# Optimization experiments

Hardware: AMD Instinct MI355X
Metric: run time of the kernel (lower is better)

Reference implementation:

```python
import jax, jax.numpy as jnp
import numpy as np

N, E, F_IN, H, D = 50000, 800000, 128, 4, 32


def setup_inputs() -> dict:
    key = jax.random.key(0)
    k_x, k_e, k_w, k_al, k_ar = jax.random.split(key, 5)
    x = jax.random.normal(k_x, (N, F_IN), dtype=jnp.float32)
    edge_index = jax.random.randint(k_e, (2, E), 0, N, dtype=jnp.int32).astype(jnp.int64)
    # xavier-uniform-like scales
    s_w = float(np.sqrt(6.0 / (F_IN + H * D)))
    s_a = float(np.sqrt(6.0 / (D + 1)))
    W = jax.random.uniform(k_w, (F_IN, H * D), jnp.float32, -s_w, s_w)
    att_l = jax.random.uniform(k_al, (H, D), jnp.float32, -s_a, s_a)
    att_r = jax.random.uniform(k_ar, (H, D), jnp.float32, -s_a, s_a)
    bias = jnp.zeros((H * D,), jnp.float32)
    return {"x": x, "edge_index": edge_index, "W": W, "att_l": att_l, "att_r": att_r, "bias": bias}


def reference(x, edge_index, W, att_l, att_r, bias):
    num_nodes = x.shape[0]
    n_heads, head_dim = att_l.shape
    h = (x @ W).reshape(num_nodes, n_heads, head_dim)          # [N,H,D]
    alpha_l = jnp.einsum('nhd,hd->nh', h, att_l)               # [N,H]
    alpha_r = jnp.einsum('nhd,hd->nh', h, att_r)               # [N,H]
    from_idx, to_idx = edge_index[0], edge_index[1]
    att = alpha_l[from_idx] + alpha_r[to_idx]                  # [E,H]
    att = jax.nn.leaky_relu(att, negative_slope=0.2)
    # segment softmax over edges grouped by destination node (shift by global
    # per-head max, exactly as the source's _softmax effectively does)
    att = att - jax.lax.stop_gradient(jnp.max(att, axis=0, keepdims=True))
    ex = jnp.exp(att)                                          # [E,H]
    denom = jax.ops.segment_sum(ex, to_idx, num_segments=num_nodes)  # [N,H]
    att_n = ex / (denom[to_idx] + 1e-9)                        # [E,H]
    # scatter-weighted aggregation: out[n] = sum_{e: to=n} att[e] * h[from[e]]
    msgs = att_n[:, :, None] * h[from_idx]                     # [E,H,D]
    out = jax.ops.segment_sum(msgs, to_idx, num_segments=num_nodes)  # [N,H,D]
    out = out.reshape(num_nodes, n_heads * head_dim) + bias
    return out
```

## Files before the change

kernel.cpp:

```cpp
#include <hip/hip_runtime.h>
#include <cstdint>

#define N_NODES 50000
#define N_EDGES 800000
#define F_IN    128
#define N_HEADS 4
#define HEAD_DIM 32
#define F_OUT   128

#define NBUCK   391
#define NPB     128
#define KA_GRID 512
#define EPB     1563
#define EPB_PAD 1568
#define REC_CAP 2560
#define STAGE_CAP REC_CAP
#define NSTRIP  (N_NODES / 16)
#define NGEMM   ((NSTRIP + 3) / 4)

typedef unsigned int uint32;
typedef unsigned short ushort;
typedef __attribute__((ext_vector_type(8))) short short8v;
typedef __attribute__((ext_vector_type(4))) float float4v;

typedef __attribute__((address_space(1))) const ushort gushort;
typedef __attribute__((address_space(3))) ushort lushort;

__device__ __forceinline__ ushort f2bf(float f) {
    uint32 u = __float_as_uint(f);
    return (ushort)((u + 0x7FFFu + ((u >> 16) & 1u)) >> 16);
}


__device__ __forceinline__ int block_scan_excl_256(int v, int* p_total)
{
    const int t = threadIdx.x, lane = t & 63, wv = t >> 6;
    int incl = v;
#pragma unroll
    for (int d = 1; d < 64; d <<= 1) {
        int u = __shfl_up(incl, d);
        if (lane >= d) incl += u;
    }
    __shared__ int wsum[4];
    if (lane == 63) wsum[wv] = incl;
    __syncthreads();
    int woff = 0;
#pragma unroll
    for (int j = 0; j < 4; ++j) {
        int s = wsum[j];
        if (j < wv) woff += s;
    }
    if (p_total) *p_total = wsum[0] + wsum[1] + wsum[2] + wsum[3];
    __syncthreads();
    return woff + incl - v;
}

__global__ __launch_bounds__(256) void k_prep(const float* __restrict__ W,
    ushort* __restrict__ WTF)
{
    const int id = blockIdx.x * 256 + threadIdx.x;
    if (id >= 32 * 64) return;
    const int tile = id >> 6, l = id & 63;
    const int q = l >> 4, c15 = l & 15;
    const int nt = tile >> 2, kt = tile & 3;
    short8v hv, lv;
#pragma unroll
    for (int j = 0; j < 8; ++j) {
        const int k = kt * 32 + q * 8 + j;
        const float w = W[k * F_OUT + nt * 16 + c15];
        const ushort hi = f2bf(w);
        const float hif = __uint_as_float((uint32)hi << 16);
        hv[j] = (short)hi;
        lv[j] = (short)f2bf(w - hif);
    }
    *(short8v*)&WTF[tile * 512 + l * 8]         = hv;
    *(short8v*)&WTF[16384 + tile * 512 + l * 8] = lv;
}

__global__ __launch_bounds__(256, 2) void k_bin_gemm(
    const int* __restrict__ ei, const float* __restrict__ x,
    const ushort* __restrict__ WTF,
    const float* __restrict__ attl, const float* __restrict__ attr,
    uint32* __restrict__ blockarr, int* __restrict__ cnts, int* __restrict__ offs,
    uint32* __restrict__ hbq, float* __restrict__ aLp, float* __restrict__ aRp)
{
    __shared__ __attribute__((aligned(16))) char lds_buf[65536];

    if (blockIdx.x < KA_GRID) {
        int*    cur = (int*)lds_buf;
        int*    off = cur + 512;
        uint32* stg = (uint32*)(off + 512);
        const int sb = blockIdx.x, t = threadIdx.x;

        cur[t] = 0; cur[t + 256] = 0;
        __syncthreads();

        const int e0 = sb * EPB;
        const int lim = min(EPB, N_EDGES - e0);
        for (int i = t; i < lim; i += 256)
            atomicAdd(&cur[ei[N_EDGES + e0 + i] >> 7], 1);
        __syncthreads();

        const int c0 = cur[2 * t], c1 = cur[2 * t + 1];
        const int ex = block_scan_excl_256(c0 + c1, nullptr);
        off[2 * t]     = ex;
        off[2 * t + 1] = ex + c0;
        __syncthreads();

        for (int bb = t; bb < NBUCK; bb += 256) {
            cnts[(size_t)bb * KA_GRID + sb] = cur[bb];
            offs[(size_t)bb * KA_GRID + sb] = off[bb];
        }
        __syncthreads();

        for (int i = t; i < lim; i += 256) {
            const int from = ei[e0 + i];
            const int to   = ei[N_EDGES + e0 + i];
            const int pos = atomicAdd(&off[to >> 7], 1);
            stg[pos] = (uint32)from | ((uint32)(to & 127) << 16);
        }
        __syncthreads();

        uint32* dst = blockarr + (size_t)sb * EPB_PAD;
        for (int i = t; i < lim; i += 256)
            dst[i] = stg[i];
        return;
    }

    const int bid   = blockIdx.x - KA_GRID;
    const int lane  = threadIdx.x & 63;
    const int wv    = threadIdx.x >> 6;
    const int q     = lane >> 4;
    const int c15   = lane & 15;

    ushort* wt = (ushort*)lds_buf;
#pragma unroll
    for (int i = 0; i < 16; ++i) {
        const int chunk = wv * 16 + i;
        __builtin_amdgcn_global_load_lds(
            (gushort*)(WTF + chunk * 512 + lane * 8),
            (lushort*)(wt + chunk * 512), 16, 0, 0);
    }
    __syncthreads();

    const int strip = bid * 4 + wv;
    if (strip >= NSTRIP) return;
    const int row0 = strip * 16;

    const float* xrow = x + (size_t)(row0 + c15) * F_IN + q * 8;
    short8v ahi[4], alo[4];
#pragma unroll
    for (int kt = 0; kt < 4; ++kt) {
        const float4 f0 = *(const float4*)(xrow + kt * 32);
        const float4 f1 = *(const float4*)(xrow + kt * 32 + 4);
        const float fs[8] = {f0.x, f0.y, f0.z, f0.w, f1.x, f1.y, f1.z, f1.w};
#pragma unroll
        for (int j = 0; j < 8; ++j) {
            const ushort hi = f2bf(fs[j]);
            const float hif = __uint_as_float((uint32)hi << 16);
            ahi[kt][j] = (short)hi;
            alo[kt][j] = (short)f2bf(fs[j] - hif);
        }
    }

    float4v acc[8];
#pragma unroll
    for (int nt = 0; nt < 8; ++nt) {
        float4v a = {0.f, 0.f, 0.f, 0.f};
#pragma unroll
        for (int kt = 0; kt < 4; ++kt) {
            const short8v bh = *(const short8v*)(wt + (nt * 4 + kt) * 512 + lane * 8);
            const short8v bl = *(const short8v*)(wt + 16384 + (nt * 4 + kt) * 512 + lane * 8);
            a = __builtin_amdgcn_mfma_f32_16x16x32_bf16(ahi[kt], bh, a, 0, 0, 0);
            a = __builtin_amdgcn_mfma_f32_16x16x32_bf16(alo[kt], bh, a, 0, 0, 0);
            a = __builtin_amdgcn_mfma_f32_16x16x32_bf16(ahi[kt], bl, a, 0, 0, 0);
        }
        acc[nt] = a;
    }

#pragma unroll
    for (int nt = 0; nt < 4; ++nt) {
#pragma unroll
        for (int r = 0; r < 4; ++r) {
            const uint32 d = (uint32)f2bf(acc[nt][r]) | ((uint32)f2bf(acc[nt + 4][r]) << 16);
            hbq[(size_t)(row0 + q * 4 + r) * 64 + nt * 16 + c15] = d;
        }
    }

    float aLacc[4][4] = {{0.f}}, aRacc[4][4] = {{0.f}};
#pragma unroll
    for (int nt = 0; nt < 8; ++nt) {
        const float alv = attl[nt * 16 + c15];
        const float arv = attr[nt * 16 + c15];
        const int hh = nt >> 1;
#pragma unroll
        for (int r = 0; r < 4; ++r) {
            aLacc[r][hh] = fmaf(acc[nt][r], alv, aLacc[r][hh]);
            aRacc[r][hh] = fmaf(acc[nt][r], arv, aRacc[r][hh]);
        }
    }
#pragma unroll
    for (int r = 0; r < 4; ++r) {
#pragma unroll
        for (int hh = 0; hh < 4; ++hh) {
            float vl = aLacc[r][hh], vr = aRacc[r][hh];
#pragma unroll
            for (int d = 1; d < 16; d <<= 1) {
                vl += __shfl_xor(vl, d);
                vr += __shfl_xor(vr, d);
            }
            if (c15 == hh) {
                const int row = row0 + q * 4 + r;
                const int pos = (hh & 1) * 2 + (hh >> 1);
                aLp[row * N_HEADS + pos] = vl;
                aRp[row * N_HEADS + pos] = vr;
            }
        }
    }
}

__global__ __launch_bounds__(256) void k_build(const uint32* __restrict__ blockarr,
    const int* __restrict__ cnts, const int* __restrict__ offs,
    int* __restrict__ count, int* __restrict__ offsets, int* __restrict__ rec_from)
{
    __shared__ uint32 stage[STAGE_CAP];
    __shared__ int hist[NPB], curn[NPB];
    const int b = blockIdx.x, t = threadIdx.x;

    int c[2], o[2];
#pragma unroll
    for (int j = 0; j < 2; ++j) {
        c[j] = cnts[(size_t)b * KA_GRID + 2 * t + j];
        o[j] = offs[(size_t)b * KA_GRID + 2 * t + j];
    }
    int total;
    int ex = block_scan_excl_256(c[0] + c[1], &total);
    if (t < NPB) hist[t] = 0;
    __syncthreads();

#pragma unroll
    for (int j = 0; j < 2; ++j) {
        const int sb = 2 * t + j;
        const uint32* src = blockarr + (size_t)sb * EPB_PAD + o[j];
        for (int i = 0; i < c[j]; ++i) {
            const int p = ex + i;
            if (p < STAGE_CAP) stage[p] = src[i];
        }
        ex += c[j];
    }
    __syncthreads();

    const int S = min(total, STAGE_CAP);
    for (int i = t; i < S; i += 256) atomicAdd(&hist[stage[i] >> 16], 1);
    __syncthreads();

    const int hv = (t < NPB) ? hist[t] : 0;
    int tot2;
    const int lo = block_scan_excl_256(hv, &tot2);
    const int rbase = b * REC_CAP;
    const int n = b * NPB + t;
    if (t < NPB && n < N_NODES) {
        count[n]   = hv;
        offsets[n] = rbase + lo;
    }
    if (t < NPB) curn[t] = lo;
    __syncthreads();

    for (int i = t; i < S; i += 256) {
        const uint32 e = stage[i];
        const int pos = atomicAdd(&curn[e >> 16], 1);
        rec_from[rbase + pos] = (int)(e & 0xFFFFu);
    }
}

__global__ __launch_bounds__(256) void k_agg(const int* __restrict__ rec_from,
    const int* __restrict__ count, const int* __restrict__ offsets,
    const float* __restrict__ aLp, const float* __restrict__ aRp,
    const uint32* __restrict__ hbq,
    const float* __restrict__ bias, float* __restrict__ out)
{
    const int lane = threadIdx.x & 63;
    const int n = blockIdx.x * 4 + (threadIdx.x >> 6);
    if (n >= N_NODES) return;
    const int cnt  = count[n];
    const int off  = offsets[n];
    const int hsel = (lane >> 5) * 2;
    const int l31  = lane & 31;
    const int gsel = lane & 32;
    const float2 arv = *(const float2*)&aRp[n * N_HEADS + hsel];
    float ax = 0.f, ay = 0.f, ds0 = 0.f, ds1 = 0.f;

    for (int base = 0; base < cnt; base += 32) {
        const int m = min(32, cnt - base);
        int vf = 0;
        float e0p = 0.f, e1p = 0.f;
        if (l31 < m) {
            vf = rec_from[off + base + l31];
            const float2 af = *(const float2*)&aLp[vf * N_HEADS + hsel];
            float t0 = af.x + arv.x; t0 = (t0 > 0.f) ? t0 : 0.2f * t0;
            float t1 = af.y + arv.y; t1 = (t1 > 0.f) ? t1 : 0.2f * t1;
            e0p = __expf(t0);
            e1p = __expf(t1);
        }
        int i = 0;
        for (; i + 8 <= m; i += 8) {
            int f[8]; uint32 h[8]; float e0[8], e1[8];
#pragma unroll
            for (int j = 0; j < 8; ++j) {
                const int s = gsel | (i + j);
                f[j]  = __shfl(vf, s);
                e0[j] = __shfl(e0p, s);
                e1[j] = __shfl(e1p, s);
            }
#pragma unroll
            for (int j = 0; j < 8; ++j) h[j] = hbq[(size_t)f[j] * 64 + lane];
#pragma unroll
            for (int j = 0; j < 8; ++j) {
                ax = fmaf(e0[j], __uint_as_float(h[j] << 16), ax);
                ay = fmaf(e1[j], __uint_as_float(h[j] & 0xFFFF0000u), ay);
                ds0 += e0[j]; ds1 += e1[j];
            }
        }
        for (; i + 4 <= m; i += 4) {
            int f[4]; uint32 h[4]; float e0[4], e1[4];
#pragma unroll
            for (int j = 0; j < 4; ++j) {
                const int s = gsel | (i + j);
                f[j]  = __shfl(vf, s);
                e0[j] = __shfl(e0p, s);
                e1[j] = __shfl(e1p, s);
            }
#pragma unroll
            for (int j = 0; j < 4; ++j) h[j] = hbq[(size_t)f[j] * 64 + lane];
#pragma unroll
            for (int j = 0; j < 4; ++j) {
                ax = fmaf(e0[j], __uint_as_float(h[j] << 16), ax);
                ay = fmaf(e1[j], __uint_as_float(h[j] & 0xFFFF0000u), ay);
                ds0 += e0[j]; ds1 += e1[j];
            }
        }
        for (; i < m; ++i) {
            const int s = gsel | i;
            const int f = __shfl(vf, s);
            const uint32 hv = hbq[(size_t)f * 64 + lane];
            const float e0 = __shfl(e0p, s), e1 = __shfl(e1p, s);
            ax = fmaf(e0, __uint_as_float(hv << 16), ax);
            ay = fmaf(e1, __uint_as_float(hv & 0xFFFF0000u), ay);
            ds0 += e0; ds1 += e1;
        }
    }
    const float inv0 = 1.0f / (ds0 + 1e-9f);
    const float inv1 = 1.0f / (ds1 + 1e-9f);
    out[n * F_OUT + lane]      = ax * inv0 + bias[lane];
    out[n * F_OUT + 64 + lane] = ay * inv1 + bias[64 + lane];
}

extern "C" void kernel_launch(void* const* d_in, const int* in_sizes, int n_in,
                              void* d_out, int out_size, void* d_ws, size_t ws_size,
                              hipStream_t stream)
{
    const float* x    = (const float*)d_in[0];
    const int*   ei   = (const int*)d_in[1];
    const float* W    = (const float*)d_in[2];
    const float* attl = (const float*)d_in[3];
    const float* attr = (const float*)d_in[4];
    const float* bias = (const float*)d_in[5];
    float* out = (float*)d_out;

    char* p = (char*)d_ws;
    auto carve = [&](size_t bytes) -> char* {
        char* q = p;
        p += (bytes + 255) & ~size_t(255);
        return q;
    };
    uint32* hbq      = (uint32*)carve((size_t)N_NODES * 64 * 4);
    uint32* blockarr = (uint32*)carve((size_t)KA_GRID * EPB_PAD * 4);
    int*    rec_from = (int*)carve((size_t)NBUCK * REC_CAP * 4);
    ushort* WTF      = (ushort*)carve(32768 * 2);
    float*  aLp      = (float*)carve((size_t)N_NODES * N_HEADS * 4);
    float*  aRp      = (float*)carve((size_t)N_NODES * N_HEADS * 4);
    int*    cnts     = (int*)carve((size_t)NBUCK * KA_GRID * 4);
    int*    offs     = (int*)carve((size_t)NBUCK * KA_GRID * 4);
    int*    count    = (int*)carve((size_t)N_NODES * 4);
    int*    offsets  = (int*)carve((size_t)N_NODES * 4);

    k_prep<<<8, 256, 0, stream>>>(W, WTF);
    k_bin_gemm<<<KA_GRID + NGEMM, 256, 0, stream>>>(ei, x, WTF,
                                                    attl, attr, blockarr,
                                                    cnts, offs,
                                                    hbq, aLp, aRp);
    k_build<<<NBUCK, 256, 0, stream>>>(blockarr, cnts, offs,
                                       count, offsets, rec_from);
    k_agg<<<(N_NODES + 3) / 4, 256, 0, stream>>>(rec_from, count, offsets,
                                                 aLp, aRp, hbq, bias, out);
}
```

Measured before the change: 154.0 us.

## Fuse CSR build and aggregation into one kernel with LDS-resident sorted edges

Merges the bucket-build and aggregation kernels into one. Buckets are halved to 64 destination nodes each, so each block sorts its edges in LDS and then aggregates its own nodes directly, with no global rec_from/count/offsets round trip and one fewer launch. The cost is fewer, larger work units per block: each wave handles 16 nodes serially, with 782 blocks instead of 12500. That may reduce latency hiding in the gather-heavy aggregation. The staging capacity also drops to 1280 edges per bucket, which could overflow if the degree distribution is skewed.

```diff
diff --git a/kernel.cpp b/kernel.cpp
--- a/kernel.cpp
+++ b/kernel.cpp
@@ -8,13 +8,12 @@
 #define HEAD_DIM 32
 #define F_OUT   128
 
-#define NBUCK   391
-#define NPB     128
+#define NBUCK   782
+#define NPB     64
 #define KA_GRID 512
 #define EPB     1563
 #define EPB_PAD 1568
-#define REC_CAP 2560
-#define STAGE_CAP REC_CAP
+#define SCAP    1280
 #define NSTRIP  (N_NODES / 16)
 #define NGEMM   ((NSTRIP + 3) / 4)
 
@@ -88,23 +87,25 @@
 
     if (blockIdx.x < KA_GRID) {
         int*    cur = (int*)lds_buf;
-        int*    off = cur + 512;
-        uint32* stg = (uint32*)(off + 512);
+        int*    off = cur + 1024;
+        uint32* stg = (uint32*)(off + 1024);
         const int sb = blockIdx.x, t = threadIdx.x;
 
-        cur[t] = 0; cur[t + 256] = 0;
+        cur[t] = 0; cur[t + 256] = 0; cur[t + 512] = 0; cur[t + 768] = 0;
         __syncthreads();
 
         const int e0 = sb * EPB;
         const int lim = min(EPB, N_EDGES - e0);
         for (int i = t; i < lim; i += 256)
-            atomicAdd(&cur[ei[N_EDGES + e0 + i] >> 7], 1);
-        __syncthreads();
-
-        const int c0 = cur[2 * t], c1 = cur[2 * t + 1];
-        const int ex = block_scan_excl_256(c0 + c1, nullptr);
-        off[2 * t]     = ex;
-        off[2 * t + 1] = ex + c0;
+            atomicAdd(&cur[ei[N_EDGES + e0 + i] >> 6], 1);
+        __syncthreads();
+
+        int c[4], s = 0;
+#pragma unroll
+        for (int j = 0; j < 4; ++j) { c[j] = cur[4 * t + j]; s += c[j]; }
+        int ex = block_scan_excl_256(s, nullptr);
+#pragma unroll
+        for (int j = 0; j < 4; ++j) { off[4 * t + j] = ex; ex += c[j]; }
         __syncthreads();
 
         for (int bb = t; bb < NBUCK; bb += 256) {
@@ -116,8 +117,8 @@
         for (int i = t; i < lim; i += 256) {
             const int from = ei[e0 + i];
             const int to   = ei[N_EDGES + e0 + i];
-            const int pos = atomicAdd(&off[to >> 7], 1);
-            stg[pos] = (uint32)from | ((uint32)(to & 127) << 16);
+            const int pos = atomicAdd(&off[to >> 6], 1);
+            stg[pos] = (uint32)from | ((uint32)(to & 63) << 16);
         }
         __syncthreads();
 
@@ -219,12 +220,15 @@
     }
 }
 
-__global__ __launch_bounds__(256) void k_build(const uint32* __restrict__ blockarr,
+__global__ __launch_bounds__(256) void k_build_agg(const uint32* __restrict__ blockarr,
     const int* __restrict__ cnts, const int* __restrict__ offs,
-    int* __restrict__ count, int* __restrict__ offsets, int* __restrict__ rec_from)
-{
-    __shared__ uint32 stage[STAGE_CAP];
-    __shared__ int hist[NPB], curn[NPB];
+    const float* __restrict__ aLp, const float* __restrict__ aRp,
+    const uint32* __restrict__ hbq,
+    const float* __restrict__ bias, float* __restrict__ out)
+{
+    __shared__ uint32 stage[SCAP];
+    __shared__ ushort sorted[SCAP];
+    __shared__ int hist[NPB], lo0[NPB], curn[NPB];
     const int b = blockIdx.x, t = threadIdx.x;
 
     int c[2], o[2];
@@ -244,115 +248,114 @@
         const uint32* src = blockarr + (size_t)sb * EPB_PAD + o[j];
         for (int i = 0; i < c[j]; ++i) {
             const int p = ex + i;
-            if (p < STAGE_CAP) stage[p] = src[i];
+            if (p < SCAP) stage[p] = src[i];
         }
         ex += c[j];
     }
     __syncthreads();
 
-    const int S = min(total, STAGE_CAP);
+    const int S = min(total, SCAP);
     for (int i = t; i < S; i += 256) atomicAdd(&hist[stage[i] >> 16], 1);
     __syncthreads();
 
-    const int hv = (t < NPB) ? hist[t] : 0;
-    int tot2;
-    const int lo = block_scan_excl_256(hv, &tot2);
-    const int rbase = b * REC_CAP;
-    const int n = b * NPB + t;
-    if (t < NPB && n < N_NODES) {
-        count[n]   = hv;
-        offsets[n] = rbase + lo;
-    }
-    if (t < NPB) curn[t] = lo;
+    if (t < NPB) {
+        const int v = hist[t];
+        int incl = v;
+#pragma unroll
+        for (int d = 1; d < 64; d <<= 1) {
+            int u = __shfl_up(incl, d);
+            if (t >= d) incl += u;
+        }
+        lo0[t]  = incl - v;
+        curn[t] = incl - v;
+    }
     __syncthreads();
 
     for (int i = t; i < S; i += 256) {
         const uint32 e = stage[i];
         const int pos = atomicAdd(&curn[e >> 16], 1);
-        rec_from[rbase + pos] = (int)(e & 0xFFFFu);
-    }
-}
-
-__global__ __launch_bounds__(256) void k_agg(const int* __restrict__ rec_from,
-    const int* __restrict__ count, const int* __restrict__ offsets,
-    const float* __restrict__ aLp, const float* __restrict__ aRp,
-    const uint32* __restrict__ hbq,
-    const float* __restrict__ bias, float* __restrict__ out)
-{
-    const int lane = threadIdx.x & 63;
-    const int n = blockIdx.x * 4 + (threadIdx.x >> 6);
-    if (n >= N_NODES) return;
-    const int cnt  = count[n];
-    const int off  = offsets[n];
+        sorted[pos] = (ushort)(e & 0xFFFFu);
+    }
+    __syncthreads();
+
+    const int lane = t & 63;
+    const int wv   = t >> 6;
     const int hsel = (lane >> 5) * 2;
     const int l31  = lane & 31;
     const int gsel = lane & 32;
-    const float2 arv = *(const float2*)&aRp[n * N_HEADS + hsel];
-    float ax = 0.f, ay = 0.f, ds0 = 0.f, ds1 = 0.f;
-
-    for (int base = 0; base < cnt; base += 32) {
-        const int m = min(32, cnt - base);
-        int vf = 0;
-        float e0p = 0.f, e1p = 0.f;
-        if (l31 < m) {
-            vf = rec_from[off + base + l31];
-            const float2 af = *(const float2*)&aLp[vf * N_HEADS + hsel];
-            float t0 = af.x + arv.x; t0 = (t0 > 0.f) ? t0 : 0.2f * t0;
-            float t1 = af.y + arv.y; t1 = (t1 > 0.f) ? t1 : 0.2f * t1;
-            e0p = __expf(t0);
-            e1p = __expf(t1);
-        }
-        int i = 0;
-        for (; i + 8 <= m; i += 8) {
-            int f[8]; uint32 h[8]; float e0[8], e1[8];
-#pragma unroll
-            for (int j = 0; j < 8; ++j) {
-                const int s = gsel | (i + j);
-                f[j]  = __shfl(vf, s);
-                e0[j] = __shfl(e0p, s);
-                e1[j] = __shfl(e1p, s);
-            }
-#pragma unroll
-            for (int j = 0; j < 8; ++j) h[j] = hbq[(size_t)f[j] * 64 + lane];
-#pragma unroll
-            for (int j = 0; j < 8; ++j) {
-                ax = fmaf(e0[j], __uint_as_float(h[j] << 16), ax);
-                ay = fmaf(e1[j], __uint_as_float(h[j] & 0xFFFF0000u), ay);
-                ds0 += e0[j]; ds1 += e1[j];
-            }
-        }
-        for (; i + 4 <= m; i += 4) {
-            int f[4]; uint32 h[4]; float e0[4], e1[4];
-#pragma unroll
-            for (int j = 0; j < 4; ++j) {
-                const int s = gsel | (i + j);
-                f[j]  = __shfl(vf, s);
-                e0[j] = __shfl(e0p, s);
-                e1[j] = __shfl(e1p, s);
-            }
-#pragma unroll
-            for (int j = 0; j < 4; ++j) h[j] = hbq[(size_t)f[j] * 64 + lane];
-#pragma unroll
-            for (int j = 0; j < 4; ++j) {
-                ax = fmaf(e0[j], __uint_as_float(h[j] << 16), ax);
-                ay = fmaf(e1[j], __uint_as_float(h[j] & 0xFFFF0000u), ay);
-                ds0 += e0[j]; ds1 += e1[j];
-            }
-        }
-        for (; i < m; ++i) {
-            const int s = gsel | i;
-            const int f = __shfl(vf, s);
-            const uint32 hv = hbq[(size_t)f * 64 + lane];
-            const float e0 = __shfl(e0p, s), e1 = __shfl(e1p, s);
-            ax = fmaf(e0, __uint_as_float(hv << 16), ax);
-            ay = fmaf(e1, __uint_as_float(hv & 0xFFFF0000u), ay);
-            ds0 += e0; ds1 += e1;
-        }
-    }
-    const float inv0 = 1.0f / (ds0 + 1e-9f);
-    const float inv1 = 1.0f / (ds1 + 1e-9f);
-    out[n * F_OUT + lane]      = ax * inv0 + bias[lane];
-    out[n * F_OUT + 64 + lane] = ay * inv1 + bias[64 + lane];
+
+    for (int ln = wv * 16; ln < wv * 16 + 16; ++ln) {
+        const int n = b * NPB + ln;
+        if (n >= N_NODES) break;
+        const int cnt  = hist[ln];
+        const int off0 = lo0[ln];
+        const float2 arv = *(const float2*)&aRp[n * N_HEADS + hsel];
+        float ax = 0.f, ay = 0.f, ds0 = 0.f, ds1 = 0.f;
+
+        for (int base = 0; base < cnt; base += 32) {
+            const int m = min(32, cnt - base);
+            int vf = 0;
+            float e0p = 0.f, e1p = 0.f;
+            if (l31 < m) {
+                vf = (int)sorted[off0 + base + l31];
+                const float2 af = *(const float2*)&aLp[vf * N_HEADS + hsel];
+                float t0 = af.x + arv.x; t0 = (t0 > 0.f) ? t0 : 0.2f * t0;
+                float t1 = af.y + arv.y; t1 = (t1 > 0.f) ? t1 : 0.2f * t1;
+                e0p = __expf(t0);
+                e1p = __expf(t1);
+            }
+            int i = 0;
+            for (; i + 8 <= m; i += 8) {
+                int f[8]; uint32 h[8]; float e0[8], e1[8];
+#pragma unroll
+                for (int j = 0; j < 8; ++j) {
+                    const int s = gsel | (i + j);
+                    f[j]  = __shfl(vf, s);
+                    e0[j] = __shfl(e0p, s);
+                    e1[j] = __shfl(e1p, s);
+                }
+#pragma unroll
+                for (int j = 0; j < 8; ++j) h[j] = hbq[(size_t)f[j] * 64 + lane];
+#pragma unroll
+                for (int j = 0; j < 8; ++j) {
+                    ax = fmaf(e0[j], __uint_as_float(h[j] << 16), ax);
+                    ay = fmaf(e1[j], __uint_as_float(h[j] & 0xFFFF0000u), ay);
+                    ds0 += e0[j]; ds1 += e1[j];
+                }
+            }
+            for (; i + 4 <= m; i += 4) {
+                int f[4]; uint32 h[4]; float e0[4], e1[4];
+#pragma unroll
+                for (int j = 0; j < 4; ++j) {
+                    const int s = gsel | (i + j);
+                    f[j]  = __shfl(vf, s);
+                    e0[j] = __shfl(e0p, s);
+                    e1[j] = __shfl(e1p, s);
+                }
+#pragma unroll
+                for (int j = 0; j < 4; ++j) h[j] = hbq[(size_t)f[j] * 64 + lane];
+#pragma unroll
+                for (int j = 0; j < 4; ++j) {
+                    ax = fmaf(e0[j], __uint_as_float(h[j] << 16), ax);
+                    ay = fmaf(e1[j], __uint_as_float(h[j] & 0xFFFF0000u), ay);
+                    ds0 += e0[j]; ds1 += e1[j];
+                }
+            }
+            for (; i < m; ++i) {
+                const int s = gsel | i;
+                const int f = __shfl(vf, s);
+                const uint32 hv = hbq[(size_t)f * 64 + lane];
+                const float e0 = __shfl(e0p, s), e1 = __shfl(e1p, s);
+                ax = fmaf(e0, __uint_as_float(hv << 16), ax);
+                ay = fmaf(e1, __uint_as_float(hv & 0xFFFF0000u), ay);
+                ds0 += e0; ds1 += e1;
+            }
+        }
+        const float inv0 = 1.0f / (ds0 + 1e-9f);
+        const float inv1 = 1.0f / (ds1 + 1e-9f);
+        out[n * F_OUT + lane]      = ax * inv0 + bias[lane];
+        out[n * F_OUT + 64 + lane] = ay * inv1 + bias[64 + lane];
+    }
 }
 
 extern "C" void kernel_launch(void* const* d_in, const int* in_sizes, int n_in,
@@ -375,22 +378,17 @@
     };
     uint32* hbq      = (uint32*)carve((size_t)N_NODES * 64 * 4);
     uint32* blockarr = (uint32*)carve((size_t)KA_GRID * EPB_PAD * 4);
-    int*    rec_from = (int*)carve((size_t)NBUCK * REC_CAP * 4);
     ushort* WTF      = (ushort*)carve(32768 * 2);
     float*  aLp      = (float*)carve((size_t)N_NODES * N_HEADS * 4);
     float*  aRp      = (float*)carve((size_t)N_NODES * N_HEADS * 4);
     int*    cnts     = (int*)carve((size_t)NBUCK * KA_GRID * 4);
     int*    offs     = (int*)carve((size_t)NBUCK * KA_GRID * 4);
-    int*    count    = (int*)carve((size_t)N_NODES * 4);
-    int*    offsets  = (int*)carve((size_t)N_NODES * 4);
 
     k_prep<<<8, 256, 0, stream>>>(W, WTF);
     k_bin_gemm<<<KA_GRID + NGEMM, 256, 0, stream>>>(ei, x, WTF,
                                                     attl, attr, blockarr,
                                                     cnts, offs,
                                                     hbq, aLp, aRp);
-    k_build<<<NBUCK, 256, 0, stream>>>(blockarr, cnts, offs,
-                                       count, offsets, rec_from);
-    k_agg<<<(N_NODES + 3) / 4, 256, 0, stream>>>(rec_from, count, offsets,
-                                                 aLp, aRp, hbq, bias, out);
-}
+    k_build_agg<<<NBUCK, 256, 0, stream>>>(blockarr, cnts, offs,
+                                           aLp, aRp, hbq, bias, out);
+}
```

New measurement: 166.7 us. 8.2% more time.
